# Kernel optimization log

Measured on AMD Instinct MI355X. Metric: run time of the kernel, lower is better.

Reference implementation:

```python
import jax, jax.numpy as jnp
import numpy as np

N_FRAMES = 500000
INPUT_LEN = 128
N_MEMORY = 64
N_CLASSES = 64


def setup_inputs() -> dict:
    key = jax.random.key(0)
    ks = jax.random.split(key, 8)
    return {
        "inputs": jax.random.normal(ks[0], (N_FRAMES, INPUT_LEN), dtype=jnp.float32),
        "targets": jax.random.randint(ks[1], (N_FRAMES,), 0, N_CLASSES, dtype=jnp.int32),
        "W_left": jax.random.normal(ks[2], (INPUT_LEN, N_MEMORY), dtype=jnp.float32) * 0.05,
        "b_left": jax.random.normal(ks[3], (N_MEMORY,), dtype=jnp.float32) * 0.05,
        "W_right": jax.random.normal(ks[4], (INPUT_LEN, N_MEMORY), dtype=jnp.float32) * 0.05,
        "b_right": jax.random.normal(ks[5], (N_MEMORY,), dtype=jnp.float32) * 0.05,
        "W_logit": jax.random.normal(ks[6], (N_MEMORY, N_CLASSES), dtype=jnp.float32) * 0.05,
        "b_logit": jax.random.normal(ks[7], (N_CLASSES,), dtype=jnp.float32) * 0.05,
    }


def reference(inputs, targets, W_left, b_left, W_right, b_right, W_logit, b_logit):
    # inputs: [T, input_len]; targets unused by forward (consumed by external CTC loss)
    left = jax.nn.sigmoid(inputs @ W_left + b_left)    # [T, M]
    right = jax.nn.sigmoid(inputs @ W_right + b_right)  # [T, M]
    prod = left * right                                  # [T, M]

    # Linear recurrence: u_0 = 0; u_t = prod[t-1] * u_{t-1} + (1 - left[t-1])
    a = prod[:-1]        # [T-1, M]
    b = 1.0 - left[:-1]  # [T-1, M]

    def step(u, ab):
        a_t, b_t = ab
        u = a_t * u + b_t
        return u, u

    u0 = jnp.zeros((left.shape[1],), dtype=left.dtype)
    _, zs = jax.lax.scan(step, u0, (a, b))
    z = jnp.concatenate([u0[None, :], zs], axis=0)  # [T, M]

    logits = z @ W_logit + b_logit  # [T, n_classes]
    return logits
```

## Files before the change

### kernel.cpp

```cpp
#include <hip/hip_runtime.h>
#include <hip/hip_fp16.h>


constexpr int NF  = 500000;
constexpr int KIN = 128;
constexpr int M   = 64;
constexpr int CH  = 64;
constexpr int NC  = (NF + CH - 1) / CH;
constexpr int NG  = (NC + 63) / 64;
constexpr int GPW = (NG + 3) / 4;
constexpr int K1GRID = 1024;

typedef _Float16 f16x8 __attribute__((ext_vector_type(8)));
typedef __fp16   fp16x2 __attribute__((ext_vector_type(2)));
typedef float    f32x4 __attribute__((ext_vector_type(4)));

__device__ __forceinline__ float sig(float x) {
    return __builtin_amdgcn_rcpf(1.0f + __expf(-x));
}

__global__ void k0_pack(const float* __restrict__ WL, const float* __restrict__ WR,
                        const float* __restrict__ WLog,
                        _Float16* __restrict__ wpre, _Float16* __restrict__ wlogpre)
{
    int flat = blockIdx.x * 1024 + threadIdx.x * 4;
    if (flat < 16384) {
        int k = flat >> 7, col = flat & 127;
        float4 v = (col < 64) ? *(const float4*)&WL[k * 64 + col]
                              : *(const float4*)&WR[k * 64 + (col - 64)];
        int kb = k >> 3, kj = k & 7;
        wpre[(kb * 128 + col + 0) * 8 + kj] = (_Float16)v.x;
        wpre[(kb * 128 + col + 1) * 8 + kj] = (_Float16)v.y;
        wpre[(kb * 128 + col + 2) * 8 + kj] = (_Float16)v.z;
        wpre[(kb * 128 + col + 3) * 8 + kj] = (_Float16)v.w;
    } else if (flat < 16384 + 4096) {
        int f2 = flat - 16384;
        int k = f2 >> 6, c = f2 & 63;
        float4 v = *(const float4*)&WLog[f2];
        int kb = k >> 3, kj = k & 7;
        wlogpre[(kb * 64 + c + 0) * 8 + kj] = (_Float16)v.x;
        wlogpre[(kb * 64 + c + 1) * 8 + kj] = (_Float16)v.y;
        wlogpre[(kb * 64 + c + 2) * 8 + kj] = (_Float16)v.z;
        wlogpre[(kb * 64 + c + 3) * 8 + kj] = (_Float16)v.w;
    }
}

__global__ __launch_bounds__(256, 4)
void k1_prefix(const float* __restrict__ X, const _Float16* __restrict__ wpre,
               const float* __restrict__ bL, const float* __restrict__ bR,
               float* __restrict__ sA, float* __restrict__ sB,
               _Float16* __restrict__ pre)
{
    __shared__ _Float16 w_s[16384];
    __shared__ float pA_s[256], pB_s[256];
    const int tid = threadIdx.x, lane = tid & 63, w = tid >> 6;
    const int arow = lane & 15, kb = lane >> 4;

    #pragma unroll
    for (int i = 0; i < 8; ++i) {
        int c16 = i * 256 + tid;
        *(f16x8*)&w_s[c16 * 8] = ((const f16x8*)wpre)[c16];
    }
    __syncthreads();

    float blv[4], brv[4];
    #pragma unroll
    for (int c = 0; c < 4; ++c) { blv[c] = bL[c * 16 + arow]; brv[c] = bR[c * 16 + arow]; }

    f32x4 xv[8];
    int cid = blockIdx.x;
    {
        const int xrow = cid * CH + w * 16 + arow;
        const float* xp = X + (size_t)xrow * KIN;
        const bool rowok = xrow < NF;
        #pragma unroll
        for (int s = 0; s < 4; ++s) {
            xv[2 * s]     = rowok ? *(const f32x4*)&xp[s * 32 + kb * 8]
                                  : (f32x4){0.f, 0.f, 0.f, 0.f};
            xv[2 * s + 1] = rowok ? *(const f32x4*)&xp[s * 32 + kb * 8 + 4]
                                  : (f32x4){0.f, 0.f, 0.f, 0.f};
        }
    }

    while (cid < NC) {
        const int t0 = cid * CH;
        const int nxt = cid + K1GRID;

        f32x4 acc[8];
        #pragma unroll
        for (int c = 0; c < 8; ++c) acc[c] = (f32x4){0.f, 0.f, 0.f, 0.f};
        #pragma unroll
        for (int s = 0; s < 4; ++s) {
            fp16x2 p0 = __builtin_amdgcn_cvt_pkrtz(xv[2 * s].x, xv[2 * s].y);
            fp16x2 p1 = __builtin_amdgcn_cvt_pkrtz(xv[2 * s].z, xv[2 * s].w);
            fp16x2 p2 = __builtin_amdgcn_cvt_pkrtz(xv[2 * s + 1].x, xv[2 * s + 1].y);
            fp16x2 p3 = __builtin_amdgcn_cvt_pkrtz(xv[2 * s + 1].z, xv[2 * s + 1].w);
            f16x8 af = { (_Float16)p0[0], (_Float16)p0[1],
                         (_Float16)p1[0], (_Float16)p1[1],
                         (_Float16)p2[0], (_Float16)p2[1],
                         (_Float16)p3[0], (_Float16)p3[1] };
            #pragma unroll
            for (int c = 0; c < 8; ++c) {
                f16x8 bf = *(const f16x8*)&w_s[((s * 4 + kb) * 128 + c * 16 + arow) * 8];
                acc[c] = __builtin_amdgcn_mfma_f32_16x16x32_f16(af, bf, acc[c], 0, 0, 0);
            }
        }

        if (nxt < NC) {
            const int xrow = nxt * CH + w * 16 + arow;
            const float* xp = X + (size_t)xrow * KIN;
            const bool rowok = xrow < NF;
            #pragma unroll
            for (int s = 0; s < 4; ++s) {
                xv[2 * s]     = rowok ? *(const f32x4*)&xp[s * 32 + kb * 8]
                                      : (f32x4){0.f, 0.f, 0.f, 0.f};
                xv[2 * s + 1] = rowok ? *(const f32x4*)&xp[s * 32 + kb * 8 + 4]
                                      : (f32x4){0.f, 0.f, 0.f, 0.f};
            }
        }

        float a[4][4], b[4][4];
        #pragma unroll
        for (int c = 0; c < 4; ++c) {
            #pragma unroll
            for (int reg = 0; reg < 4; ++reg) {
                float lv = sig(acc[c][reg] + blv[c]);
                float rv = sig(acc[c + 4][reg] + brv[c]);
                a[c][reg] = lv * rv;
                b[c][reg] = 1.0f - lv;
            }
        }

        float Ai[4], Bi[4];
        #pragma unroll
        for (int c = 0; c < 4; ++c) {
            float A = 1.f, B = 0.f;
            #pragma unroll
            for (int reg = 0; reg < 4; ++reg) {
                if (t0 + w * 16 + kb * 4 + reg < NF - 1) {
                    B = fmaf(a[c][reg], B, b[c][reg]);
                    A *= a[c][reg];
                }
            }
            Ai[c] = A; Bi[c] = B;
        }
        #pragma unroll
        for (int d = 16; d < 64; d <<= 1) {
            #pragma unroll
            for (int c = 0; c < 4; ++c) {
                float pA = __shfl_up(Ai[c], d), pB = __shfl_up(Bi[c], d);
                if (lane >= d) { Bi[c] = fmaf(Ai[c], pB, Bi[c]); Ai[c] *= pA; }
            }
        }

        float eA[4], eB[4];
        #pragma unroll
        for (int c = 0; c < 4; ++c) {
            eA[c] = __shfl_up(Ai[c], 16);
            eB[c] = __shfl_up(Bi[c], 16);
            if (kb == 0) { eA[c] = 1.f; eB[c] = 0.f; }
        }
        if (kb == 3) {
            #pragma unroll
            for (int c = 0; c < 4; ++c) {
                pA_s[w * 64 + c * 16 + arow] = Ai[c];
                pB_s[w * 64 + c * 16 + arow] = Bi[c];
            }
        }
        __syncthreads();

        float EA[4] = {1.f, 1.f, 1.f, 1.f}, EB[4] = {0.f, 0.f, 0.f, 0.f};
        for (int s2 = 0; s2 < w; ++s2) {
            #pragma unroll
            for (int c = 0; c < 4; ++c) {
                float qa = pA_s[s2 * 64 + c * 16 + arow];
                float qb = pB_s[s2 * 64 + c * 16 + arow];
                EB[c] = fmaf(qa, EB[c], qb);
                EA[c] *= qa;
            }
        }
        _Float16* prebase = pre + (size_t)cid * 8192;
        #pragma unroll
        for (int c = 0; c < 4; ++c) {
            float pa = eA[c] * EA[c];
            float pb = fmaf(eA[c], EB[c], eB[c]);
            f16x8 sv;
            #pragma unroll
            for (int reg = 0; reg < 4; ++reg) {
                fp16x2 pp = __builtin_amdgcn_cvt_pkrtz(pa, pb);
                sv[2 * reg]     = (_Float16)pp[0];
                sv[2 * reg + 1] = (_Float16)pp[1];
                if (t0 + w * 16 + kb * 4 + reg < NF - 1) {
                    pb = fmaf(a[c][reg], pb, b[c][reg]);
                    pa *= a[c][reg];
                }
            }
            *(f16x8*)&prebase[((((w * 4 + kb) * 4 + c) * 16 + arow) * 4) * 2] = sv;
        }
        if (tid < 64) {
            float At = 1.f, Bt = 0.f;
            #pragma unroll
            for (int s2 = 0; s2 < 4; ++s2) {
                float qa = pA_s[s2 * 64 + tid], qb = pB_s[s2 * 64 + tid];
                Bt = fmaf(qa, Bt, qb);
                At *= qa;
            }
            sA[tid * NC + cid] = At;
            sB[tid * NC + cid] = Bt;
        }
        __syncthreads();
        cid = nxt;
    }
}

__global__ __launch_bounds__(256)
void k3_scan(const float* __restrict__ sA, const float* __restrict__ sB,
             float* __restrict__ u0)
{
    __shared__ float tA_s[4], tB_s[4];
    const int j    = blockIdx.x;
    const int lane = threadIdx.x & 63;
    const int w    = threadIdx.x >> 6;

    float PA[GPW], PB[GPW];
    float cA = 1.f, cB = 0.f;
    #pragma unroll
    for (int g = 0; g < GPW; ++g) {
        int c = (w * GPW + g) * 64 + lane;
        float A = 1.f, B = 0.f;
        if (c < NC) { A = sA[j * NC + c]; B = sB[j * NC + c]; }
        #pragma unroll
        for (int d = 1; d < 64; d <<= 1) {
            float pA = __shfl_up(A, d), pB = __shfl_up(B, d);
            if (lane >= d) { B = fmaf(A, pB, B); A *= pA; }
        }
        float eA = __shfl_up(A, 1), eB = __shfl_up(B, 1);
        if (lane == 0) { eA = 1.f; eB = 0.f; }
        PA[g] = eA * cA;
        PB[g] = fmaf(eA, cB, eB);
        float tA = __shfl(A, 63), tB = __shfl(B, 63);
        cB = fmaf(tA, cB, tB);
        cA *= tA;
    }
    if (lane == 0) { tA_s[w] = cA; tB_s[w] = cB; }
    __syncthreads();
    float uw = 0.f;
    for (int s2 = 0; s2 < w; ++s2) uw = fmaf(tA_s[s2], uw, tB_s[s2]);
    #pragma unroll
    for (int g = 0; g < GPW; ++g) {
        int c = (w * GPW + g) * 64 + lane;
        if (c < NC) u0[c * M + j] = fmaf(PA[g], uw, PB[g]);
    }
}

__global__ __launch_bounds__(256, 8)
void k4_light(const _Float16* __restrict__ pre, const float* __restrict__ u0,
              const _Float16* __restrict__ wlogpre, const float* __restrict__ bLog,
              float* __restrict__ out)
{
    __shared__ _Float16 z_s[64 * 72];
    const int tid = threadIdx.x, lane = tid & 63, w = tid >> 6;
    const int arow = lane & 15, kb = lane >> 4;
    const int t0 = blockIdx.x * CH;

    float u0v[4];
    #pragma unroll
    for (int c = 0; c < 4; ++c) u0v[c] = u0[blockIdx.x * 64 + c * 16 + arow];

    const _Float16* prebase = pre + (size_t)blockIdx.x * 8192;
    #pragma unroll
    for (int c = 0; c < 4; ++c) {
        f16x8 pv = __builtin_nontemporal_load(
            (const f16x8*)&prebase[((((w * 4 + kb) * 4 + c) * 16 + arow) * 4) * 2]);
        #pragma unroll
        for (int reg = 0; reg < 4; ++reg) {
            int rl = w * 16 + kb * 4 + reg;
            float z = fmaf((float)pv[2 * reg], u0v[c], (float)pv[2 * reg + 1]);
            z_s[rl * 72 + c * 16 + arow] = (_Float16)z;
        }
    }
    __syncthreads();

    f32x4 acc2[4];
    #pragma unroll
    for (int ct = 0; ct < 4; ++ct) acc2[ct] = (f32x4){0.f, 0.f, 0.f, 0.f};
    #pragma unroll
    for (int ks = 0; ks < 2; ++ks) {
        f16x8 af = *(const f16x8*)&z_s[(w * 16 + arow) * 72 + ks * 32 + kb * 8];
        #pragma unroll
        for (int ct = 0; ct < 4; ++ct) {
            f16x8 bf = *(const f16x8*)&wlogpre[((ks * 4 + kb) * 64 + ct * 16 + arow) * 8];
            acc2[ct] = __builtin_amdgcn_mfma_f32_16x16x32_f16(af, bf, acc2[ct], 0, 0, 0);
        }
    }
    #pragma unroll
    for (int ct = 0; ct < 4; ++ct) {
        float bv = bLog[ct * 16 + arow];
        #pragma unroll
        for (int reg = 0; reg < 4; ++reg) {
            int t = t0 + w * 16 + kb * 4 + reg;
            if (t < NF)
                __builtin_nontemporal_store(acc2[ct][reg] + bv,
                                            &out[t * M + ct * 16 + arow]);
        }
    }
}

extern "C" void kernel_launch(void* const* d_in, const int* in_sizes, int n_in,
                              void* d_out, int out_size, void* d_ws, size_t ws_size,
                              hipStream_t stream)
{
    const float* X    = (const float*)d_in[0];
    const float* WL   = (const float*)d_in[2];
    const float* bL   = (const float*)d_in[3];
    const float* WR   = (const float*)d_in[4];
    const float* bR   = (const float*)d_in[5];
    const float* WLog = (const float*)d_in[6];
    const float* bLog = (const float*)d_in[7];

    _Float16* pre = (_Float16*)d_ws;
    float* sA = (float*)((char*)d_ws + (size_t)NC * 8192 * 2);
    float* sB = sA + (size_t)64 * NC;
    float* u0 = sB + (size_t)64 * NC;
    _Float16* wpre    = (_Float16*)(u0 + (size_t)64 * NC);
    _Float16* wlogpre = wpre + 16384;

    k0_pack<<<20, 256, 0, stream>>>(WL, WR, WLog, wpre, wlogpre);
    k1_prefix<<<K1GRID, 256, 0, stream>>>(X, wpre, bL, bR, sA, sB, pre);
    k3_scan<<<M, 256, 0, stream>>>(sA, sB, u0);
    k4_light<<<NC, 256, 0, stream>>>(pre, u0, wlogpre, bLog, (float*)d_out);
}
```

Before: 159.4 us.

## Process two chunks per 512-thread block in k1 and drop register prefetch

The prefix kernel now uses 512-thread blocks, where each half of the block handles its own 64-row chunk. This halves the per-chunk cost of staging the shared weights and raises occupancy, with launch bounds now asking for 6 blocks. The software prefetch of the next chunk's X rows into registers is removed, which frees registers but stops overlapping loads with the MFMA work. The grid drops to 768 blocks walking over chunk pairs.

Result: slower. 177.8 us (+11.5%).

```diff
diff --git a/kernel.cpp b/kernel.cpp
--- a/kernel.cpp
+++ b/kernel.cpp
@@ -7,9 +7,10 @@
 constexpr int M   = 64;
 constexpr int CH  = 64;
 constexpr int NC  = (NF + CH - 1) / CH;
+constexpr int NPAIR = (NC + 1) / 2;
 constexpr int NG  = (NC + 63) / 64;
 constexpr int GPW = (NG + 3) / 4;
-constexpr int K1GRID = 1024;
+constexpr int K1BLOCKS = 768;
 
 typedef _Float16 f16x8 __attribute__((ext_vector_type(8)));
 typedef __fp16   fp16x2 __attribute__((ext_vector_type(2)));
@@ -45,20 +46,24 @@
     }
 }
 
-__global__ __launch_bounds__(256, 4)
+__global__ __launch_bounds__(512, 6)
 void k1_prefix(const float* __restrict__ X, const _Float16* __restrict__ wpre,
                const float* __restrict__ bL, const float* __restrict__ bR,
                float* __restrict__ sA, float* __restrict__ sB,
                _Float16* __restrict__ pre)
 {
     __shared__ _Float16 w_s[16384];
-    __shared__ float pA_s[256], pB_s[256];
-    const int tid = threadIdx.x, lane = tid & 63, w = tid >> 6;
+    __shared__ float pA_s[512], pB_s[512];
+    const int tid  = threadIdx.x;
+    const int lane = tid & 63;
+    const int wall = tid >> 6;
+    const int w    = wall & 3;
+    const int half = wall >> 2;
     const int arow = lane & 15, kb = lane >> 4;
 
     #pragma unroll
-    for (int i = 0; i < 8; ++i) {
-        int c16 = i * 256 + tid;
+    for (int i = 0; i < 4; ++i) {
+        int c16 = i * 512 + tid;
         *(f16x8*)&w_s[c16 * 8] = ((const f16x8*)wpre)[c16];
     }
     __syncthreads();
@@ -67,12 +72,15 @@
     #pragma unroll
     for (int c = 0; c < 4; ++c) { blv[c] = bL[c * 16 + arow]; brv[c] = bR[c * 16 + arow]; }
 
-    f32x4 xv[8];
-    int cid = blockIdx.x;
-    {
-        const int xrow = cid * CH + w * 16 + arow;
+    for (int pair = blockIdx.x; pair < NPAIR; pair += K1BLOCKS) {
+        const int cid = 2 * pair + half;
+        const bool valid = cid < NC;
+        const int t0 = cid * CH;
+
+        const int xrow = t0 + w * 16 + arow;
         const float* xp = X + (size_t)xrow * KIN;
-        const bool rowok = xrow < NF;
+        const bool rowok = valid && (xrow < NF);
+        f32x4 xv[8];
         #pragma unroll
         for (int s = 0; s < 4; ++s) {
             xv[2 * s]     = rowok ? *(const f32x4*)&xp[s * 32 + kb * 8]
@@ -80,12 +88,6 @@
             xv[2 * s + 1] = rowok ? *(const f32x4*)&xp[s * 32 + kb * 8 + 4]
                                   : (f32x4){0.f, 0.f, 0.f, 0.f};
         }
-    }
-
-    while (cid < NC) {
-        const int t0 = cid * CH;
-        const int nxt = cid + K1GRID;
-
         f32x4 acc[8];
         #pragma unroll
         for (int c = 0; c < 8; ++c) acc[c] = (f32x4){0.f, 0.f, 0.f, 0.f};
@@ -106,19 +108,6 @@
             }
         }
 
-        if (nxt < NC) {
-            const int xrow = nxt * CH + w * 16 + arow;
-            const float* xp = X + (size_t)xrow * KIN;
-            const bool rowok = xrow < NF;
-            #pragma unroll
-            for (int s = 0; s < 4; ++s) {
-                xv[2 * s]     = rowok ? *(const f32x4*)&xp[s * 32 + kb * 8]
-                                      : (f32x4){0.f, 0.f, 0.f, 0.f};
-                xv[2 * s + 1] = rowok ? *(const f32x4*)&xp[s * 32 + kb * 8 + 4]
-                                      : (f32x4){0.f, 0.f, 0.f, 0.f};
-            }
-        }
-
         float a[4][4], b[4][4];
         #pragma unroll
         for (int c = 0; c < 4; ++c) {
@@ -163,8 +152,8 @@
         if (kb == 3) {
             #pragma unroll
             for (int c = 0; c < 4; ++c) {
-                pA_s[w * 64 + c * 16 + arow] = Ai[c];
-                pB_s[w * 64 + c * 16 + arow] = Bi[c];
+                pA_s[half * 256 + w * 64 + c * 16 + arow] = Ai[c];
+                pB_s[half * 256 + w * 64 + c * 16 + arow] = Bi[c];
             }
         }
         __syncthreads();
@@ -173,43 +162,45 @@
         for (int s2 = 0; s2 < w; ++s2) {
             #pragma unroll
             for (int c = 0; c < 4; ++c) {
-                float qa = pA_s[s2 * 64 + c * 16 + arow];
-                float qb = pB_s[s2 * 64 + c * 16 + arow];
+                float qa = pA_s[half * 256 + s2 * 64 + c * 16 + arow];
+                float qb = pB_s[half * 256 + s2 * 64 + c * 16 + arow];
                 EB[c] = fmaf(qa, EB[c], qb);
                 EA[c] *= qa;
             }
         }
-        _Float16* prebase = pre + (size_t)cid * 8192;
-        #pragma unroll
-        for (int c = 0; c < 4; ++c) {
-            float pa = eA[c] * EA[c];
-            float pb = fmaf(eA[c], EB[c], eB[c]);
-            f16x8 sv;
-            #pragma unroll
-            for (int reg = 0; reg < 4; ++reg) {
-                fp16x2 pp = __builtin_amdgcn_cvt_pkrtz(pa, pb);
-                sv[2 * reg]     = (_Float16)pp[0];
-                sv[2 * reg + 1] = (_Float16)pp[1];
-                if (t0 + w * 16 + kb * 4 + reg < NF - 1) {
-                    pb = fmaf(a[c][reg], pb, b[c][reg]);
-                    pa *= a[c][reg];
+        if (valid) {
+            _Float16* prebase = pre + (size_t)cid * 8192;
+            #pragma unroll
+            for (int c = 0; c < 4; ++c) {
+                float pa = eA[c] * EA[c];
+                float pb = fmaf(eA[c], EB[c], eB[c]);
+                f16x8 sv;
+                #pragma unroll
+                for (int reg = 0; reg < 4; ++reg) {
+                    fp16x2 pp = __builtin_amdgcn_cvt_pkrtz(pa, pb);
+                    sv[2 * reg]     = (_Float16)pp[0];
+                    sv[2 * reg + 1] = (_Float16)pp[1];
+                    if (t0 + w * 16 + kb * 4 + reg < NF - 1) {
+                        pb = fmaf(a[c][reg], pb, b[c][reg]);
+                        pa *= a[c][reg];
+                    }
                 }
-            }
-            *(f16x8*)&prebase[((((w * 4 + kb) * 4 + c) * 16 + arow) * 4) * 2] = sv;
-        }
-        if (tid < 64) {
+                *(f16x8*)&prebase[((((w * 4 + kb) * 4 + c) * 16 + arow) * 4) * 2] = sv;
+            }
+        }
+        if (w == 0 && valid) {
             float At = 1.f, Bt = 0.f;
             #pragma unroll
             for (int s2 = 0; s2 < 4; ++s2) {
-                float qa = pA_s[s2 * 64 + tid], qb = pB_s[s2 * 64 + tid];
+                float qa = pA_s[half * 256 + s2 * 64 + lane];
+                float qb = pB_s[half * 256 + s2 * 64 + lane];
                 Bt = fmaf(qa, Bt, qb);
                 At *= qa;
             }
-            sA[tid * NC + cid] = At;
-            sB[tid * NC + cid] = Bt;
+            sA[lane * NC + cid] = At;
+            sB[lane * NC + cid] = Bt;
         }
         __syncthreads();
-        cid = nxt;
     }
 }
 
@@ -326,7 +317,7 @@
     _Float16* wlogpre = wpre + 16384;
 
     k0_pack<<<20, 256, 0, stream>>>(WL, WR, WLog, wpre, wlogpre);
-    k1_prefix<<<K1GRID, 256, 0, stream>>>(X, wpre, bL, bR, sA, sB, pre);
+    k1_prefix<<<K1BLOCKS, 512, 0, stream>>>(X, wpre, bL, bR, sA, sB, pre);
     k3_scan<<<M, 256, 0, stream>>>(sA, sB, u0);
     k4_light<<<NC, 256, 0, stream>>>(pre, u0, wlogpre, bLog, (float*)d_out);
 }
```
